# Kernel tuning notes

Measured on AMD Instinct MI355X. Metric: run time of the kernel, lower is better.

## Reference

```python
import jax, jax.numpy as jnp
from jax import lax
import numpy as np

N, BITS, NCLS = 2048, 64, 100
LAMBDA = 1.0
ALPHA = 1.0


def setup_inputs() -> dict:
    key = jax.random.key(0)
    ku, kl = jax.random.split(key)
    u = jax.random.normal(ku, (N, BITS), dtype=jnp.float32)
    labels = jax.random.randint(kl, (N,), 0, NCLS)
    y = jax.nn.one_hot(labels, NCLS, dtype=jnp.float32)  # [N, C]
    return {"u": u, "y": y}


def reference(u, y):
    # inner_product[i, j] = <u_i, u_j>;  s[i, j] = (y_i . y_j > 0)
    ip = u @ u.T                      # [N, N]
    s = (y @ y.T) > 0                 # [N, N] bool

    def step(carry, xs):
        tot, cnt = carry
        ip_row, s_row = xs            # [N], [N]
        pos = s_row
        neg = ~s_row
        # triple[p, n] = ip[p] - ip[n] - ALPHA, clamped like the original
        T = jnp.clip(ip_row[:, None] - ip_row[None, :] - ALPHA, -100.0, 50.0)
        # -(T - log(1 + exp(T))) = softplus(T) - T
        L = jax.nn.softplus(T) - T    # [N, N]
        pm = (pos[:, None] & neg[None, :]).astype(L.dtype)
        npairs = pm.sum()
        valid = (pos.sum() > 0) & (neg.sum() > 0)
        row_loss = jnp.where(valid, (L * pm).sum() / jnp.maximum(npairs, 1.0), 0.0)
        return (tot + row_loss, cnt + valid.astype(jnp.float32)), None

    (tot, cnt), _ = lax.scan(step, (jnp.float32(0.0), jnp.float32(0.0)), (ip, s))
    loss1 = jnp.where(cnt > 0, tot / jnp.maximum(cnt, 1.0), 0.0)
    loss2 = LAMBDA * jnp.mean((u - jnp.sign(u)) ** 2)
    return loss1 + loss2
```

## Files before the change

kernel.cpp:

```cpp
#include <hip/hip_runtime.h>
#include <hip/hip_bf16.h>
#include <math.h>

#define NROWS 2048
#define BITS  64
#define NCLS  100
#define ALPHA_C  1.0f
#define LAMBDA_C 1.0f
#define ECLAMP   1.0e9f
#define RPB      4
#define NPMAX    64

typedef __bf16 bf16x8 __attribute__((ext_vector_type(8)));
typedef float  floatx4 __attribute__((ext_vector_type(4)));


__device__ __forceinline__ float block_reduce_sum(float v, float* wsum) {
    __syncthreads();
    #pragma unroll
    for (int off = 32; off > 0; off >>= 1) v += __shfl_down(v, off);
    int tid = threadIdx.x;
    if ((tid & 63) == 0) wsum[tid >> 6] = v;
    __syncthreads();
    float r = 0.f;
    if (tid == 0) {
        #pragma unroll
        for (int w = 0; w < 4; ++w) r += wsum[w];
    }
    return r;
}

__device__ __forceinline__ float softplus_mt(float T) {
    return fmaxf(-T, 0.f) + __logf(1.f + __expf(-fabsf(T)));
}


__global__ __launch_bounds__(256) void prep_kernel(const float* __restrict__ u,
                                                   const float* __restrict__ y,
                                                   unsigned short* __restrict__ ub,
                                                   unsigned char* __restrict__ lab8,
                                                   float* __restrict__ qp) {
    const int tid = threadIdx.x;
    if (blockIdx.x < 64) {
        __shared__ float wsum[4];
        const int base = blockIdx.x * 2048 + tid * 8;
        float4 v0 = *(const float4*)(u + base);
        float4 v1 = *(const float4*)(u + base + 4);
        float vv[8] = {v0.x, v0.y, v0.z, v0.w, v1.x, v1.y, v1.z, v1.w};
        unsigned short ob[8];
        float q = 0.f;
        #pragma unroll
        for (int m = 0; m < 8; ++m) {
            const float v = vv[m];
            const float sg = (v > 0.f) ? 1.f : ((v < 0.f) ? -1.f : 0.f);
            const float d = v - sg;
            q = fmaf(d, d, q);
            __hip_bfloat16 h = __float2bfloat16(v);
            ob[m] = *reinterpret_cast<unsigned short*>(&h);
        }
        *(uint4*)(ub + base) = *(const uint4*)ob;
        float t = block_reduce_sum(q, wsum);
        if (tid == 0) qp[blockIdx.x] = t;
    } else {
        const int bi = blockIdx.x - 64;
        const int row = bi * 4 + (tid >> 6);
        const int lane = tid & 63;
        const float* yr = y + (size_t)row * NCLS;
        float v0 = yr[lane];
        float v1 = (lane < NCLS - 64) ? yr[lane + 64] : 0.f;
        unsigned long long m0 = __ballot(v0 > 0.5f);
        unsigned long long m1 = __ballot(v1 > 0.5f);
        if (lane == 0) {
            int c = m0 ? (__ffsll(m0) - 1) : (m1 ? 64 + __ffsll(m1) - 1 : 0);
            lab8[row] = (unsigned char)c;
        }
    }
}

__global__ __launch_bounds__(256, 2) void fused_kernel(const unsigned short* __restrict__ ub,
                                                       const unsigned char* __restrict__ lab8,
                                                       float* __restrict__ rl,
                                                       float* __restrict__ vl) {
    __shared__ float slab[RPB][NROWS];
    alignas(16) __shared__ float ap[RPB][NPMAX];
    __shared__ unsigned char labL[NROWS];
    __shared__ int np_s[RPB];
    __shared__ float wsum[RPB][4];

    const int tid  = threadIdx.x;
    const int wave = tid >> 6;
    const int lane = tid & 63;
    const int r0     = blockIdx.x * RPB;
    const int i0     = (blockIdx.x >> 2) * 16;
    const int myquad = blockIdx.x & 3;

    ((uint2*)labL)[tid] = ((const uint2*)lab8)[tid];
    if (tid < RPB) np_s[tid] = 0;

    const int rsel = lane & 15;
    const int quad = lane >> 4;
    const int koff = quad * 8;
    uint4 a0r = *(const uint4*)(ub + (size_t)(i0 + rsel) * BITS + koff);
    uint4 a1r = *(const uint4*)(ub + (size_t)(i0 + rsel) * BITS + 32 + koff);
    bf16x8 A0 = __builtin_bit_cast(bf16x8, a0r);
    bf16x8 A1 = __builtin_bit_cast(bf16x8, a1r);

    for (int jt = wave * 32; jt < wave * 32 + 32; ++jt) {
        const int j0 = jt * 16;
        const int jr = j0 + rsel;
        uint4 b0r = *(const uint4*)(ub + (size_t)jr * BITS + koff);
        uint4 b1r = *(const uint4*)(ub + (size_t)jr * BITS + 32 + koff);
        bf16x8 B0 = __builtin_bit_cast(bf16x8, b0r);
        bf16x8 B1 = __builtin_bit_cast(bf16x8, b1r);
        floatx4 c = {0.f, 0.f, 0.f, 0.f};
        c = __builtin_amdgcn_mfma_f32_16x16x32_bf16(A0, B0, c, 0, 0, 0);
        c = __builtin_amdgcn_mfma_f32_16x16x32_bf16(A1, B1, c, 0, 0, 0);
        if (quad == myquad) {
            #pragma unroll
            for (int r = 0; r < 4; ++r)
                slab[r][j0 + rsel] = c[r];
        }
    }
    __syncthreads();

    int crow[RPB];
    #pragma unroll
    for (int r = 0; r < RPB; ++r) crow[r] = labL[r0 + r];
    #pragma unroll
    for (int r = 0; r < RPB; ++r) {
        const int cr = crow[r];
        #pragma unroll
        for (int m = 0; m < 8; ++m) {
            const int j = tid + m * 256;
            if (labL[j] == cr) {
                int slot = atomicAdd(&np_s[r], 1);
                if (slot < NPMAX)
                    ap[r][slot] = fminf(__expf(-slab[r][j]), ECLAMP);
            }
        }
    }
    __syncthreads();
    int npcap[RPB], npr[RPB];
    #pragma unroll
    for (int r = 0; r < RPB; ++r) {
        npcap[r] = (np_s[r] < NPMAX) ? np_s[r] : NPMAX;
        npr[r] = (npcap[r] + 3) & ~3;
    }
    if (tid < RPB) {
        for (int k = npcap[tid]; k < npr[tid]; ++k) ap[tid][k] = 0.f;
    }
    __syncthreads();

    float srow[RPB];
    #pragma unroll
    for (int r = 0; r < RPB; ++r) {
        const int cr = crow[r];
        float Eb[8];
        #pragma unroll
        for (int m = 0; m < 8; ++m) {
            const int j = tid + m * 256;
            const float g = slab[r][j];
            Eb[m] = (labL[j] == cr) ? 0.f : fminf(__expf(g + ALPHA_C), ECLAMP);
        }
        float s0 = 0.f, s1 = 0.f, s2 = 0.f, s3 = 0.f;
        for (int k = 0; k < npr[r]; k += 4) {
            const float4 e = *(const float4*)(&ap[r][k]);
            #pragma unroll
            for (int m = 0; m < 8; m += 2) {
                const float q0 = Eb[m], q1 = Eb[m + 1];
                const float f0 = fmaf(q0, e.x, 1.f);
                const float f1 = fmaf(q0, e.y, 1.f);
                const float f2 = fmaf(q0, e.z, 1.f);
                const float f3 = fmaf(q0, e.w, 1.f);
                s0 += __log2f(f0 * f1);
                s1 += __log2f(f2 * f3);
                const float g0 = fmaf(q1, e.x, 1.f);
                const float g1 = fmaf(q1, e.y, 1.f);
                const float g2 = fmaf(q1, e.z, 1.f);
                const float g3 = fmaf(q1, e.w, 1.f);
                s2 += __log2f(g0 * g1);
                s3 += __log2f(g2 * g3);
            }
        }
        srow[r] = (s0 + s1) + (s2 + s3);
    }

    #pragma unroll
    for (int r = 0; r < RPB; ++r) {
        #pragma unroll
        for (int off = 32; off > 0; off >>= 1)
            srow[r] += __shfl_down(srow[r], off);
    }
    if (lane == 0) {
        #pragma unroll
        for (int r = 0; r < RPB; ++r) wsum[r][wave] = srow[r];
    }
    __syncthreads();
    if (tid < RPB) {
        const float ln2 = 0.6931471805599453f;
        const float tot = ((wsum[tid][0] + wsum[tid][1]) +
                           (wsum[tid][2] + wsum[tid][3])) * ln2;
        const int np = np_s[tid];
        const int nneg = NROWS - np;
        const int valid = (np > 0 && nneg > 0) ? 1 : 0;
        rl[r0 + tid] = valid ? (tot / fmaxf((float)np * (float)nneg, 1.f)) : 0.f;
        vl[r0 + tid] = (float)valid;
    }
}

__global__ __launch_bounds__(256) void finalize2_kernel(const float* __restrict__ rl,
                                                        const float* __restrict__ vl,
                                                        const float* __restrict__ qp,
                                                        float* __restrict__ out) {
    __shared__ float wsum[4];
    const int tid = threadIdx.x;
    float t = 0.f, v = 0.f;
    for (int idx = tid; idx < NROWS; idx += 256) { t += rl[idx]; v += vl[idx]; }
    float q = (tid < 64) ? qp[tid] : 0.f;
    float tt = block_reduce_sum(t, wsum);
    float vv = block_reduce_sum(v, wsum);
    float qq = block_reduce_sum(q, wsum);
    if (tid == 0) {
        const float loss1 = (vv > 0.f) ? (tt / fmaxf(vv, 1.f)) : 0.f;
        const float loss2 = LAMBDA_C * (qq / (float)(NROWS * BITS));
        out[0] = loss1 + loss2;
    }
}


__global__ __launch_bounds__(256) void labels_only_kernel(const float* __restrict__ y,
                                                          int* __restrict__ labels) {
    const int tid = threadIdx.x;
    const int row = blockIdx.x * 4 + (tid >> 6);
    const int lane = tid & 63;
    const float* yr = y + (size_t)row * NCLS;
    float v0 = yr[lane];
    float v1 = (lane < NCLS - 64) ? yr[lane + 64] : 0.f;
    unsigned long long m0 = __ballot(v0 > 0.5f);
    unsigned long long m1 = __ballot(v1 > 0.5f);
    if (lane == 0) {
        int c = m0 ? (__ffsll(m0) - 1) : (m1 ? 64 + __ffsll(m1) - 1 : 0);
        labels[row] = c;
    }
}

__global__ __launch_bounds__(256) void row_loss_kernel(const float* __restrict__ u,
                                                       const int* __restrict__ labels,
                                                       float* __restrict__ acc) {
    __shared__ float a[NROWS];
    __shared__ float apv[NROWS];
    __shared__ int lab[NROWS];
    __shared__ float ui[BITS];
    __shared__ int npos_s;
    __shared__ float wsum[4];

    const int i = blockIdx.x;
    const int tid = threadIdx.x;

    if (tid < BITS) ui[tid] = u[(size_t)i * BITS + tid];
    if (tid == 0) npos_s = 0;
    __syncthreads();

    #pragma unroll
    for (int m = 0; m < NROWS / 256; ++m) {
        const int j = tid + m * 256;
        const float4* uj = (const float4*)(u + (size_t)j * BITS);
        float s0 = 0.f, s1 = 0.f, s2 = 0.f, s3 = 0.f;
        #pragma unroll
        for (int q = 0; q < BITS / 4; ++q) {
            float4 v = uj[q];
            s0 = fmaf(v.x, ui[4 * q + 0], s0);
            s1 = fmaf(v.y, ui[4 * q + 1], s1);
            s2 = fmaf(v.z, ui[4 * q + 2], s2);
            s3 = fmaf(v.w, ui[4 * q + 3], s3);
        }
        a[j] = (s0 + s1) + (s2 + s3);
        lab[j] = labels[j];
    }
    __syncthreads();

    const int c = lab[i];
    #pragma unroll
    for (int m = 0; m < NROWS / 256; ++m) {
        const int j = tid + m * 256;
        if (lab[j] == c) { int k = atomicAdd(&npos_s, 1); apv[k] = a[j]; }
    }
    __syncthreads();
    const int npos = npos_s;
    const int nneg = NROWS - npos;

    float b[NROWS / 256];
    #pragma unroll
    for (int m = 0; m < NROWS / 256; ++m) {
        const int j = tid + m * 256;
        b[m] = (lab[j] != c) ? (a[j] + ALPHA_C) : -3.0e38f;
    }

    float lsum = 0.f;
    for (int k = 0; k < npos; ++k) {
        const float apk = apv[k];
        #pragma unroll
        for (int m = 0; m < NROWS / 256; ++m) lsum += softplus_mt(apk - b[m]);
    }

    float tot = block_reduce_sum(lsum, wsum);
    if (tid == 0) {
        const int valid = (npos > 0 && nneg > 0) ? 1 : 0;
        const float npairs = fmaxf((float)npos * (float)nneg, 1.f);
        const float rlv = valid ? (tot / npairs) : 0.f;
        atomicAdd(&acc[0], rlv);
        atomicAdd(&acc[1], (float)valid);
    }
}

__global__ __launch_bounds__(256) void quant_kernel(const float* __restrict__ u,
                                                    float* __restrict__ acc) {
    __shared__ float wsum[4];
    const int stride = gridDim.x * 256;
    float s = 0.f;
    for (int t = blockIdx.x * 256 + threadIdx.x; t < NROWS * BITS; t += stride) {
        float v = u[t];
        float sg = (v > 0.f) ? 1.f : ((v < 0.f) ? -1.f : 0.f);
        float d = v - sg;
        s = fmaf(d, d, s);
    }
    float tot = block_reduce_sum(s, wsum);
    if (threadIdx.x == 0) atomicAdd(&acc[2], tot);
}

__global__ void finalize_kernel(const float* __restrict__ acc,
                                float* __restrict__ out) {
    const float tot = acc[0], cnt = acc[1], q = acc[2];
    const float loss1 = (cnt > 0.f) ? (tot / fmaxf(cnt, 1.f)) : 0.f;
    const float loss2 = LAMBDA_C * (q / (float)(NROWS * BITS));
    out[0] = loss1 + loss2;
}


extern "C" void kernel_launch(void* const* d_in, const int* in_sizes, int n_in,
                              void* d_out, int out_size, void* d_ws, size_t ws_size,
                              hipStream_t stream) {
    const float* u = (const float*)d_in[0];
    const float* y = (const float*)d_in[1];
    float* out = (float*)d_out;

    unsigned char* lab8 = (unsigned char*)d_ws;
    float* rl = (float*)((char*)d_ws + 8192);
    float* vl = (float*)((char*)d_ws + 16384);
    float* qp = (float*)((char*)d_ws + 24576);
    unsigned short* ub = (unsigned short*)((char*)d_ws + 32768);
    const size_t NEED = 32768 + (size_t)NROWS * BITS * sizeof(unsigned short);

    if (ws_size >= NEED) {
        prep_kernel<<<576, 256, 0, stream>>>(u, y, ub, lab8, qp);
        fused_kernel<<<NROWS / RPB, 256, 0, stream>>>(ub, lab8, rl, vl);
        finalize2_kernel<<<1, 256, 0, stream>>>(rl, vl, qp, out);
    } else {
        float* acc2 = (float*)d_ws;
        int*   lab2 = (int*)((char*)d_ws + 256);
        hipMemsetAsync(d_ws, 0, 256, stream);
        labels_only_kernel<<<512, 256, 0, stream>>>(y, lab2);
        row_loss_kernel<<<NROWS, 256, 0, stream>>>(u, lab2, acc2);
        quant_kernel<<<64, 256, 0, stream>>>(u, acc2);
        finalize_kernel<<<1, 1, 0, stream>>>(acc2, out);
    }
}
```

Measured before the change: 89.95 us.

## Split row-loss work across j-quarters with atomic accumulation and fp32 positive dots

The fused kernel is restructured so each block handles 4 rows against a quarter of the columns. This gives 2048 blocks instead of 512, with no 32KB slab in LDS and higher occupancy. Partial row sums are combined through global atomicAdd into rl, which prep_kernel now zeroes, and per-row positive counts go to a new npg buffer used by a reworked finalize kernel. Positive-pair exponentials are recomputed from fp32 u dot products, so every block sees all positives regardless of its column quarter. The cost is redundant positive-pair work per quarter, plus atomics and dependence on zero-initialisation ordering.

```diff
diff --git a/kernel.cpp b/kernel.cpp
--- a/kernel.cpp
+++ b/kernel.cpp
@@ -8,8 +8,8 @@
 #define ALPHA_C  1.0f
 #define LAMBDA_C 1.0f
 #define ECLAMP   1.0e9f
-#define RPB      4
 #define NPMAX    64
+#define APSTRIDE 68
 
 typedef __bf16 bf16x8 __attribute__((ext_vector_type(8)));
 typedef float  floatx4 __attribute__((ext_vector_type(4)));
@@ -39,7 +39,8 @@
                                                    const float* __restrict__ y,
                                                    unsigned short* __restrict__ ub,
                                                    unsigned char* __restrict__ lab8,
-                                                   float* __restrict__ qp) {
+                                                   float* __restrict__ qp,
+                                                   float* __restrict__ rl) {
     const int tid = threadIdx.x;
     if (blockIdx.x < 64) {
         __shared__ float wsum[4];
@@ -63,6 +64,7 @@
         if (tid == 0) qp[blockIdx.x] = t;
     } else {
         const int bi = blockIdx.x - 64;
+        if (tid == 0) ((float4*)rl)[bi] = make_float4(0.f, 0.f, 0.f, 0.f);
         const int row = bi * 4 + (tid >> 6);
         const int lane = tid & 63;
         const float* yr = y + (size_t)row * NCLS;
@@ -77,36 +79,45 @@
     }
 }
 
-__global__ __launch_bounds__(256, 2) void fused_kernel(const unsigned short* __restrict__ ub,
+__global__ __launch_bounds__(256, 4) void evalj_kernel(const unsigned short* __restrict__ ub,
+                                                       const float* __restrict__ u,
                                                        const unsigned char* __restrict__ lab8,
                                                        float* __restrict__ rl,
-                                                       float* __restrict__ vl) {
-    __shared__ float slab[RPB][NROWS];
-    alignas(16) __shared__ float ap[RPB][NPMAX];
+                                                       int* __restrict__ npg) {
     __shared__ unsigned char labL[NROWS];
-    __shared__ int np_s[RPB];
-    __shared__ float wsum[RPB][4];
+    __shared__ float uloc[4][BITS];
+    alignas(16) __shared__ float ap[4][APSTRIDE];
+    __shared__ int np_s[4];
+    __shared__ float wsum[4][4];
 
     const int tid  = threadIdx.x;
     const int wave = tid >> 6;
     const int lane = tid & 63;
-    const int r0     = blockIdx.x * RPB;
-    const int i0     = (blockIdx.x >> 2) * 16;
-    const int myquad = blockIdx.x & 3;
-
-    ((uint2*)labL)[tid] = ((const uint2*)lab8)[tid];
-    if (tid < RPB) np_s[tid] = 0;
-
     const int rsel = lane & 15;
     const int quad = lane >> 4;
     const int koff = quad * 8;
+    const int b     = blockIdx.x;
+    const int i0    = (b >> 4) * 16;
+    const int rblk  = (b >> 2) & 3;
+    const int jbase = (b & 3) * 512;
+
+    ((uint2*)labL)[tid] = ((const uint2*)lab8)[tid];
+    {
+        const int q = tid >> 6, k = tid & 63;
+        uloc[q][k] = u[(size_t)(i0 + 4 * q + rblk) * BITS + k];
+    }
+    for (int k = tid; k < 4 * APSTRIDE; k += 256) ((float*)ap)[k] = 0.f;
+    if (tid < 4) np_s[tid] = 0;
+
     uint4 a0r = *(const uint4*)(ub + (size_t)(i0 + rsel) * BITS + koff);
     uint4 a1r = *(const uint4*)(ub + (size_t)(i0 + rsel) * BITS + 32 + koff);
     bf16x8 A0 = __builtin_bit_cast(bf16x8, a0r);
     bf16x8 A1 = __builtin_bit_cast(bf16x8, a1r);
 
-    for (int jt = wave * 32; jt < wave * 32 + 32; ++jt) {
-        const int j0 = jt * 16;
+    float g[8];
+    #pragma unroll
+    for (int t = 0; t < 8; ++t) {
+        const int j0 = jbase + (wave * 8 + t) * 16;
         const int jr = j0 + rsel;
         uint4 b0r = *(const uint4*)(ub + (size_t)jr * BITS + koff);
         uint4 b1r = *(const uint4*)(ub + (size_t)jr * BITS + 32 + koff);
@@ -115,107 +126,104 @@
         floatx4 c = {0.f, 0.f, 0.f, 0.f};
         c = __builtin_amdgcn_mfma_f32_16x16x32_bf16(A0, B0, c, 0, 0, 0);
         c = __builtin_amdgcn_mfma_f32_16x16x32_bf16(A1, B1, c, 0, 0, 0);
-        if (quad == myquad) {
-            #pragma unroll
-            for (int r = 0; r < 4; ++r)
-                slab[r][j0 + rsel] = c[r];
-        }
-    }
-    __syncthreads();
-
-    int crow[RPB];
-    #pragma unroll
-    for (int r = 0; r < RPB; ++r) crow[r] = labL[r0 + r];
-    #pragma unroll
-    for (int r = 0; r < RPB; ++r) {
-        const int cr = crow[r];
-        #pragma unroll
-        for (int m = 0; m < 8; ++m) {
-            const int j = tid + m * 256;
-            if (labL[j] == cr) {
-                int slot = atomicAdd(&np_s[r], 1);
-                if (slot < NPMAX)
-                    ap[r][slot] = fminf(__expf(-slab[r][j]), ECLAMP);
+        g[t] = (rblk == 0) ? c[0] : (rblk == 1) ? c[1] : (rblk == 2) ? c[2] : c[3];
+    }
+    __syncthreads();
+
+    int crow[4];
+    #pragma unroll
+    for (int q = 0; q < 4; ++q) crow[q] = labL[i0 + 4 * q + rblk];
+    #pragma unroll
+    for (int m = 0; m < 8; ++m) {
+        const int j = tid + m * 256;
+        const int lj = labL[j];
+        #pragma unroll
+        for (int q = 0; q < 4; ++q) {
+            if (lj == crow[q]) {
+                int slot = atomicAdd(&np_s[q], 1);
+                if (slot < NPMAX) {
+                    const float4* uj4 = (const float4*)(u + (size_t)j * BITS);
+                    float s0 = 0.f, s1 = 0.f, s2 = 0.f, s3 = 0.f;
+                    #pragma unroll
+                    for (int kk = 0; kk < BITS / 4; ++kk) {
+                        float4 vj = uj4[kk];
+                        s0 = fmaf(vj.x, uloc[q][4 * kk + 0], s0);
+                        s1 = fmaf(vj.y, uloc[q][4 * kk + 1], s1);
+                        s2 = fmaf(vj.z, uloc[q][4 * kk + 2], s2);
+                        s3 = fmaf(vj.w, uloc[q][4 * kk + 3], s3);
+                    }
+                    ap[q][slot] = fminf(__expf(-((s0 + s1) + (s2 + s3))), ECLAMP);
+                }
             }
         }
     }
     __syncthreads();
-    int npcap[RPB], npr[RPB];
-    #pragma unroll
-    for (int r = 0; r < RPB; ++r) {
-        npcap[r] = (np_s[r] < NPMAX) ? np_s[r] : NPMAX;
-        npr[r] = (npcap[r] + 3) & ~3;
-    }
-    if (tid < RPB) {
-        for (int k = npcap[tid]; k < npr[tid]; ++k) ap[tid][k] = 0.f;
-    }
-    __syncthreads();
-
-    float srow[RPB];
-    #pragma unroll
-    for (int r = 0; r < RPB; ++r) {
-        const int cr = crow[r];
-        float Eb[8];
-        #pragma unroll
-        for (int m = 0; m < 8; ++m) {
-            const int j = tid + m * 256;
-            const float g = slab[r][j];
-            Eb[m] = (labL[j] == cr) ? 0.f : fminf(__expf(g + ALPHA_C), ECLAMP);
-        }
-        float s0 = 0.f, s1 = 0.f, s2 = 0.f, s3 = 0.f;
-        for (int k = 0; k < npr[r]; k += 4) {
-            const float4 e = *(const float4*)(&ap[r][k]);
-            #pragma unroll
-            for (int m = 0; m < 8; m += 2) {
-                const float q0 = Eb[m], q1 = Eb[m + 1];
-                const float f0 = fmaf(q0, e.x, 1.f);
-                const float f1 = fmaf(q0, e.y, 1.f);
-                const float f2 = fmaf(q0, e.z, 1.f);
-                const float f3 = fmaf(q0, e.w, 1.f);
-                s0 += __log2f(f0 * f1);
-                s1 += __log2f(f2 * f3);
-                const float g0 = fmaf(q1, e.x, 1.f);
-                const float g1 = fmaf(q1, e.y, 1.f);
-                const float g2 = fmaf(q1, e.z, 1.f);
-                const float g3 = fmaf(q1, e.w, 1.f);
-                s2 += __log2f(g0 * g1);
-                s3 += __log2f(g2 * g3);
-            }
-        }
-        srow[r] = (s0 + s1) + (s2 + s3);
-    }
-
-    #pragma unroll
-    for (int r = 0; r < RPB; ++r) {
-        #pragma unroll
-        for (int off = 32; off > 0; off >>= 1)
-            srow[r] += __shfl_down(srow[r], off);
-    }
-    if (lane == 0) {
-        #pragma unroll
-        for (int r = 0; r < RPB; ++r) wsum[r][wave] = srow[r];
-    }
-    __syncthreads();
-    if (tid < RPB) {
+
+    int npmx = np_s[0];
+    npmx = (np_s[1] > npmx) ? np_s[1] : npmx;
+    npmx = (np_s[2] > npmx) ? np_s[2] : npmx;
+    npmx = (np_s[3] > npmx) ? np_s[3] : npmx;
+    npmx = (npmx > NPMAX) ? NPMAX : npmx;
+    const int npr = (npmx + 3) & ~3;
+
+    const int myLab = labL[i0 + 4 * quad + rblk];
+    float Eb[8];
+    #pragma unroll
+    for (int t = 0; t < 8; ++t) {
+        const int j = jbase + (wave * 8 + t) * 16 + rsel;
+        Eb[t] = (labL[j] == myLab) ? 0.f : fminf(__expf(g[t] + ALPHA_C), ECLAMP);
+    }
+
+    float s0 = 0.f, s1 = 0.f, s2 = 0.f, s3 = 0.f;
+    for (int k = 0; k < npr; k += 4) {
+        const float4 e = *(const float4*)(&ap[quad][k]);
+        #pragma unroll
+        for (int t = 0; t < 8; t += 2) {
+            const float q0 = Eb[t], q1 = Eb[t + 1];
+            const float f0 = fmaf(q0, e.x, 1.f);
+            const float f1 = fmaf(q0, e.y, 1.f);
+            const float f2 = fmaf(q0, e.z, 1.f);
+            const float f3 = fmaf(q0, e.w, 1.f);
+            s0 += __log2f(f0 * f1);
+            s1 += __log2f(f2 * f3);
+            const float g0 = fmaf(q1, e.x, 1.f);
+            const float g1 = fmaf(q1, e.y, 1.f);
+            const float g2 = fmaf(q1, e.z, 1.f);
+            const float g3 = fmaf(q1, e.w, 1.f);
+            s2 += __log2f(g0 * g1);
+            s3 += __log2f(g2 * g3);
+        }
+    }
+    float srow = (s0 + s1) + (s2 + s3);
+
+    #pragma unroll
+    for (int off = 1; off < 16; off <<= 1) srow += __shfl_xor(srow, off);
+    if (rsel == 0) wsum[quad][wave] = srow;
+    __syncthreads();
+    if (tid < 4) {
         const float ln2 = 0.6931471805599453f;
         const float tot = ((wsum[tid][0] + wsum[tid][1]) +
                            (wsum[tid][2] + wsum[tid][3])) * ln2;
-        const int np = np_s[tid];
-        const int nneg = NROWS - np;
-        const int valid = (np > 0 && nneg > 0) ? 1 : 0;
-        rl[r0 + tid] = valid ? (tot / fmaxf((float)np * (float)nneg, 1.f)) : 0.f;
-        vl[r0 + tid] = (float)valid;
-    }
-}
-
-__global__ __launch_bounds__(256) void finalize2_kernel(const float* __restrict__ rl,
-                                                        const float* __restrict__ vl,
+        const int row = i0 + 4 * tid + rblk;
+        atomicAdd(&rl[row], tot);
+        npg[row] = np_s[tid];
+    }
+}
+
+__global__ __launch_bounds__(256) void finalize3_kernel(const float* __restrict__ rl,
+                                                        const int* __restrict__ npg,
                                                         const float* __restrict__ qp,
                                                         float* __restrict__ out) {
     __shared__ float wsum[4];
     const int tid = threadIdx.x;
     float t = 0.f, v = 0.f;
-    for (int idx = tid; idx < NROWS; idx += 256) { t += rl[idx]; v += vl[idx]; }
+    for (int row = tid; row < NROWS; row += 256) {
+        const int np = npg[row];
+        const int nneg = NROWS - np;
+        const int valid = (np > 0 && nneg > 0) ? 1 : 0;
+        t += valid ? (rl[row] / fmaxf((float)np * (float)nneg, 1.f)) : 0.f;
+        v += (float)valid;
+    }
     float q = (tid < 64) ? qp[tid] : 0.f;
     float tt = block_reduce_sum(t, wsum);
     float vv = block_reduce_sum(v, wsum);
@@ -345,16 +353,16 @@
     float* out = (float*)d_out;
 
     unsigned char* lab8 = (unsigned char*)d_ws;
-    float* rl = (float*)((char*)d_ws + 8192);
-    float* vl = (float*)((char*)d_ws + 16384);
-    float* qp = (float*)((char*)d_ws + 24576);
+    float* rl  = (float*)((char*)d_ws + 8192);
+    int*   npg = (int*)((char*)d_ws + 16384);
+    float* qp  = (float*)((char*)d_ws + 24576);
     unsigned short* ub = (unsigned short*)((char*)d_ws + 32768);
     const size_t NEED = 32768 + (size_t)NROWS * BITS * sizeof(unsigned short);
 
     if (ws_size >= NEED) {
-        prep_kernel<<<576, 256, 0, stream>>>(u, y, ub, lab8, qp);
-        fused_kernel<<<NROWS / RPB, 256, 0, stream>>>(ub, lab8, rl, vl);
-        finalize2_kernel<<<1, 256, 0, stream>>>(rl, vl, qp, out);
+        prep_kernel<<<576, 256, 0, stream>>>(u, y, ub, lab8, qp, rl);
+        evalj_kernel<<<2048, 256, 0, stream>>>(ub, u, lab8, rl, npg);
+        finalize3_kernel<<<1, 256, 0, stream>>>(rl, npg, qp, out);
     } else {
         float* acc2 = (float*)d_ws;
         int*   lab2 = (int*)((char*)d_ws + 256);
```

New measurement: 150.4 us. 67.2% more time.
